# Performance work log

Hardware: AMD Instinct MI355X
Metric: run time of the kernel (lower is better)

The kernel has to match this reference:

```python
import jax, jax.numpy as jnp
import numpy as np

B = 32; N = 512; SEQ_LEN = 8
L = 0.05; T_REF = 5.0; V_TH = 20.0; V_RES = 0.0
SQL = float(np.sqrt(L))
BN_EPS = 1e-5

# ---- Dawson-style lookup tables for the LIF moment activation (built once, float64) ----
_XG = np.linspace(-10.0, 4.0, 7001)
_DX = _XG[1] - _XG[0]

def _cumtrapz(y):
    return np.concatenate([[0.0], np.cumsum(0.5 * (y[1:] + y[:-1]) * _DX)])

_phi = np.exp(-_XG ** 2)
_I = np.exp(-100.0) / 20.0 + _cumtrapz(_phi)          # int_{-inf}^x e^{-t^2} dt (asymptotic tail at -10)
_g = np.exp(_XG ** 2) * _I                             # 1st Dawson-like function g(x)
_G = _cumtrapz(_g)                                     # int g dx (rel. to -10)
_h = np.exp(_XG ** 2) * _cumtrapz(_phi * _g ** 2)      # 2nd Dawson-like function h(x)
_H = _cumtrapz(_h)                                     # int h dx

XG = jnp.asarray(_XG, jnp.float32)
GT = jnp.asarray(_g, jnp.float32)
GI = jnp.asarray(_G, jnp.float32)
HI = jnp.asarray(_H, jnp.float32)

def _interp(x, tab):
    return jnp.interp(x, XG, tab)

def moment_activate(u, s, rho):
    # Mnn_Activate_Mean / Std / Corr: LIF moment activation
    s = jnp.maximum(s, 1e-6)
    ub = jnp.clip((V_TH * L - u) / (s * SQL), -10.0, 4.0)
    lb = jnp.clip((V_RES * L - u) / (s * SQL), -10.0, 4.0)
    dG = _interp(ub, GI) - _interp(lb, GI)
    ua = 1.0 / (T_REF + (2.0 / L) * dG)                               # mean firing rate
    dH = jnp.maximum(_interp(ub, HI) - _interp(lb, HI), 0.0)
    sa = jnp.sqrt((8.0 / L ** 2) * dH * ua ** 3)                      # firing std
    dg = _interp(ub, GT) - _interp(lb, GT)
    chi = ua ** 2 * (2.0 / L) * dg / (SQL * jnp.maximum(sa, 1e-9))    # linear response coeff
    eye = jnp.eye(rho.shape[-1], dtype=rho.dtype)
    rho_out = chi[:, :, None] * chi[:, None, :] * rho                 # [B,N,N]
    rho_out = rho_out * (1.0 - eye) + eye                             # unit diagonal
    return ua, sa, rho_out

def linear_corr(W, b, u, s, rho):
    # Mnn_Linear_Corr: mean via affine map, covariance via W C W^T
    u_out = u @ W.T + b
    Cin = rho * s[:, :, None] * s[:, None, :]                         # [B,N,N] covariance
    C = jnp.einsum('bik,lk->bil', jnp.einsum('ij,bjk->bik', W, Cin), W)
    var = jnp.clip(jnp.diagonal(C, axis1=1, axis2=2), 0.0, None)
    s_out = jnp.sqrt(var)
    denom = s_out[:, :, None] * s_out[:, None, :]
    rho_out = jnp.where(denom > 1e-12, C / jnp.maximum(denom, 1e-12), 0.0)
    return u_out, s_out, rho_out

def mexi_hat(n, k=0.3):
    dx = 2.0 * np.pi / n
    x = np.arange(0.0, 2.0 * np.pi, dx)[:n]
    y = np.exp(2.0 * (np.cos(x) - 1.0)) * np.cos(2.0 * x)
    j = np.arange(n)
    idx = (j[None, :] - j[:, None]) % n                               # w[i,:] = y.roll(i)
    return y[idx].astype(np.float32)

def setup_inputs() -> dict:
    ks = jax.random.split(jax.random.key(0), 10)
    u = jax.random.normal(ks[0], (B, N), jnp.float32)
    s = jax.random.uniform(ks[1], (B, N), jnp.float32, 0.1, 1.0)
    A = jax.random.normal(ks[2], (B, N, N), jnp.float32) / np.sqrt(N)
    sym = 0.5 * (A + jnp.swapaxes(A, 1, 2))
    eye = jnp.eye(N, dtype=jnp.float32)
    rho = jnp.clip(sym, -0.5, 0.5) * (1.0 - eye) + eye                # valid-ish corr matrix
    u_ext = jax.random.normal(ks[3], (B, N), jnp.float32)
    s_ext = jax.random.uniform(ks[4], (B, N), jnp.float32, 0.1, 1.0)
    W = 0.02 * jax.random.normal(ks[5], (N, N), jnp.float32) + 0.1 * jnp.asarray(mexi_hat(N))
    b = 0.02 * jax.random.normal(ks[6], (N,), jnp.float32)
    W_ext = 0.02 * jax.random.normal(ks[7], (N, N), jnp.float32)
    b_ext = 0.02 * jax.random.normal(ks[8], (N,), jnp.float32)
    w_mean = 2.5 * jnp.ones((N,), jnp.float32)
    b_mean = 2.5 * jnp.ones((N,), jnp.float32)
    w_mean_ext = 2.5 * jnp.ones((N,), jnp.float32)
    b_mean_ext = 2.5 * jnp.ones((N,), jnp.float32)
    return {'u': u, 's': s, 'rho': rho, 'u_ext': u_ext, 's_ext': s_ext,
            'W': W, 'b': b, 'W_ext': W_ext, 'b_ext': b_ext,
            'w_mean': w_mean, 'b_mean': b_mean,
            'w_mean_ext': w_mean_ext, 'b_mean_ext': b_mean_ext,
            'seq_len': SEQ_LEN}

def reference(u, s, rho, u_ext, s_ext, W, b, W_ext, b_ext,
              w_mean, b_mean, w_mean_ext, b_mean_ext, seq_len):
    # external pathway (Mnn_Linear_without_Corr + BN), computed once
    u_e = u_ext @ W_ext.T + b_ext
    s_e = jnp.sqrt((s_ext ** 2) @ (W_ext ** 2).T)
    mean_e = jnp.mean(u_e, axis=0); var_e = jnp.var(u_e, axis=0)
    f_e = w_mean_ext / jnp.sqrt(var_e + BN_EPS)
    s_e = s_e * jnp.abs(f_e)                                          # Mnn_Std_Bn1d (uses pre-BN stats)
    u_e = (u_e - mean_e) * f_e + b_mean_ext

    def step(carry, _):
        u, s, rho = carry
        u, s, rho = linear_corr(W, b, u, s, rho)
        mean = jnp.mean(u, axis=0); var = jnp.var(u, axis=0)
        f = w_mean / jnp.sqrt(var + BN_EPS)
        s = s * jnp.abs(f)
        u = (u - mean) * f + b_mean
        u = u + u_e
        s = jnp.sqrt(s * s + s_e * s_e)
        return moment_activate(u, s, rho), None

    (u, s, rho), _ = jax.lax.scan(step, (u, s, rho), None, length=seq_len)
    return u, s, rho
```

## Files before the change

kernel.cpp:

```cpp
#include <hip/hip_runtime.h>
#include <math.h>


#define BB 32
#define NN 512
#define SEQ 8
#define TG 7001

typedef float f32x4 __attribute__((ext_vector_type(4)));
typedef short s16x8 __attribute__((ext_vector_type(8)));

#define GL16(g, l) __builtin_amdgcn_global_load_lds( \
    (const __attribute__((address_space(1))) void*)(g), \
    (__attribute__((address_space(3))) void*)(l), 16, 0, 0)

__device__ __forceinline__ unsigned short bf16_rne(float v) {
    unsigned u = __float_as_uint(v);
    u += 0x7FFFu + ((u >> 16) & 1u);
    return (unsigned short)(u >> 16);
}
__device__ __forceinline__ float bf16_f(unsigned short h) {
    return __uint_as_float(((unsigned)h) << 16);
}
__device__ __forceinline__ void split2(float v, unsigned short& h, unsigned short& l) {
    unsigned short hh = bf16_rne(v);
    h = hh;
    l = bf16_rne(v - bf16_f(hh));
}

__device__ __forceinline__ float interp_tab(const float* __restrict__ tab, float x) {
    float t = (x + 10.0f) * 500.0f;
    t = fminf(fmaxf(t, 0.0f), 7000.0f);
    int i0 = (int)t;
    if (i0 > 6999) i0 = 6999;
    float fr = t - (float)i0;
    float a = tab[i0];
    float b = tab[i0 + 1];
    return a + fr * (b - a);
}

__global__ void k_exp(double* __restrict__ expP, double* __restrict__ expM) {
    int k = blockIdx.x * 256 + threadIdx.x;
    if (k >= TG) return;
    double x = -10.0 + (14.0 / 7000.0) * k;
    expP[k] = exp(x * x);
    expM[k] = exp(-x * x);
}

__device__ double blk_exscan(double part, double* wsum) {
    int t = threadIdx.x, lane = t & 63, wid = t >> 6;
    double run = part;
    #pragma unroll
    for (int off = 1; off < 64; off <<= 1) {
        double nv = __shfl_up(run, off);
        if (lane >= off) run += nv;
    }
    if (lane == 63) wsum[wid] = run;
    __syncthreads();
    if (t < 16) {
        double v = wsum[t];
        #pragma unroll
        for (int off = 1; off < 16; off <<= 1) {
            double nv = __shfl_up(v, off);
            if (lane >= off) v += nv;
        }
        wsum[t] = v;
    }
    __syncthreads();
    double base = (wid > 0) ? wsum[wid - 1] : 0.0;
    double ex = base + run - part;
    __syncthreads();
    return ex;
}

__global__ __launch_bounds__(1024)
void k_scan(const double* __restrict__ expP, const double* __restrict__ expM,
            float* __restrict__ GT, float* __restrict__ GI, float* __restrict__ HI) {
    __shared__ double ys[7008];
    __shared__ double wsum[16];
    const int t = threadIdx.x;
    const double dx = 14.0 / 7000.0;
    int k0 = t * 7, k1 = k0 + 7;
    if (k1 > TG) k1 = TG;
    if (k0 > TG) k0 = TG;
    int kls = (k0 < 1) ? 1 : k0;

    for (int k = k0; k < k1; ++k) ys[k] = expM[k];
    __syncthreads();

    double tmp[7];
    {
        double part = 0.0;
        for (int k = kls; k < k1; ++k) part += 0.5 * (ys[k - 1] + ys[k]) * dx;
        double run = blk_exscan(part, wsum) + exp(-100.0) / 20.0;
        int c = 0;
        for (int k = k0; k < k1; ++k) {
            if (k >= 1) run += 0.5 * (ys[k - 1] + ys[k]) * dx;
            tmp[c] = expP[k] * run;
            GT[k] = (float)tmp[c];
            ++c;
        }
        __syncthreads();
        c = 0;
        for (int k = k0; k < k1; ++k) ys[k] = tmp[c++];
        __syncthreads();
    }
    {
        double part = 0.0;
        for (int k = kls; k < k1; ++k) part += 0.5 * (ys[k - 1] + ys[k]) * dx;
        double run = blk_exscan(part, wsum);
        for (int k = k0; k < k1; ++k) {
            if (k >= 1) run += 0.5 * (ys[k - 1] + ys[k]) * dx;
            GI[k] = (float)run;
        }
        __syncthreads();
    }
    {
        double part = 0.0;
        for (int k = kls; k < k1; ++k) {
            double ya = expM[k - 1] * ys[k - 1] * ys[k - 1];
            double yb = expM[k] * ys[k] * ys[k];
            part += 0.5 * (ya + yb) * dx;
        }
        double run = blk_exscan(part, wsum);
        int c = 0;
        for (int k = k0; k < k1; ++k) {
            if (k >= 1) {
                double ya = expM[k - 1] * ys[k - 1] * ys[k - 1];
                double yb = expM[k] * ys[k] * ys[k];
                run += 0.5 * (ya + yb) * dx;
            }
            tmp[c++] = run;
        }
        __syncthreads();
        c = 0;
        for (int k = k0; k < k1; ++k) ys[k] = tmp[c++];
        __syncthreads();
    }
    {
        double part = 0.0;
        for (int k = kls; k < k1; ++k)
            part += 0.5 * (expP[k - 1] * ys[k - 1] + expP[k] * ys[k]) * dx;
        double run = blk_exscan(part, wsum);
        for (int k = k0; k < k1; ++k) {
            if (k >= 1) run += 0.5 * (expP[k - 1] * ys[k - 1] + expP[k] * ys[k]) * dx;
            HI[k] = (float)run;
        }
    }
}

__global__ void k_splitW(const float* __restrict__ W,
                         unsigned short* __restrict__ Wh, unsigned short* __restrict__ Wl) {
    int idx = blockIdx.x * 256 + threadIdx.x;
    unsigned short h, l;
    split2(W[idx], h, l);
    Wh[idx] = h; Wl[idx] = l;
}

__global__ void k_splitQ(const float* __restrict__ rho, const float* __restrict__ s,
                         unsigned short* __restrict__ Qh, unsigned short* __restrict__ Ql) {
    size_t idx = (size_t)blockIdx.x * 256 + threadIdx.x;
    int b = (int)(idx >> 18);
    int i = (int)((idx >> 9) & 511);
    int j = (int)(idx & 511);
    float v = rho[idx] * s[b * NN + i] * s[b * NN + j];
    unsigned short h, l;
    split2(v, h, l);
    Qh[idx] = h; Ql[idx] = l;
}

template <int PHASE>
__global__ __launch_bounds__(256)
void gemm_step(const unsigned short* __restrict__ Ah, const unsigned short* __restrict__ Al,
               long aStride,
               const unsigned short* __restrict__ Bh, const unsigned short* __restrict__ Bl,
               long bStride,
               unsigned short* __restrict__ Oh, unsigned short* __restrict__ Ol,
               float* __restrict__ Of,
               const float* __restrict__ Wf, float* __restrict__ sv_a, float* __restrict__ sv_b,
               const float* __restrict__ u_prev, const float* __restrict__ bvec,
               float* __restrict__ u_lin,
               const float* __restrict__ bn_w, const float* __restrict__ bmv,
               const float* __restrict__ u_e, const float* __restrict__ s_e2,
               const float* __restrict__ GT, const float* __restrict__ GI,
               const float* __restrict__ HI,
               float* __restrict__ u_next, float* __restrict__ s_next) {
    __shared__ __align__(16) unsigned short As0[8192], As1[8192], Bs0[8192], Bs1[8192];
    __shared__ float slS[256], chS[256], snS[256];

    const int id = blockIdx.x;
    const int member = (id >> 3) & 3;
    const int g = (id & 7) | ((id >> 5) << 3);
    const int p = g & 3;
    const int b = g >> 2;
    const int xt = (PHASE == 0) ? p : member;
    const int yt = (PHASE == 0) ? member : p;
    const int i0 = yt * 128, j0 = xt * 128;
    const int tid = threadIdx.x;
    const int w = tid >> 6, lane = tid & 63;
    const int wqm = w >> 1, wqn = w & 1;

    const unsigned short* Abh = Ah + (size_t)b * aStride;
    const unsigned short* Abl = Al + (size_t)b * aStride;
    const unsigned short* Bbh = Bh + (size_t)b * bStride;
    const unsigned short* Bbl = Bl + (size_t)b * bStride;

    const size_t lgoff = ((size_t)(lane >> 3) * NN) + (size_t)(((lane & 7) ^ (lane >> 3)) << 3);

    auto stage = [&](int k0) {
        #pragma unroll
        for (int inst = 0; inst < 4; ++inst) {
            const int br = w * 32 + inst * 8;
            GL16(Abh + (size_t)(i0 + br) * NN + k0 + lgoff, As0 + br * 64);
            GL16(Abl + (size_t)(i0 + br) * NN + k0 + lgoff, As1 + br * 64);
            GL16(Bbh + (size_t)(j0 + br) * NN + k0 + lgoff, Bs0 + br * 64);
            GL16(Bbl + (size_t)(j0 + br) * NN + k0 + lgoff, Bs1 + br * 64);
        }
    };
    stage(0);

    if (PHASE == 0) {
        if (xt == 0) {
            const int row = i0 + (tid >> 1);
            const int half = tid & 1;
            const float4* wr = (const float4*)(Wf + (size_t)row * NN + half * 256);
            const float4* ur = (const float4*)(u_prev + b * NN + half * 256);
            float a0 = 0.f, a1 = 0.f, a2 = 0.f, a3 = 0.f;
            #pragma unroll 8
            for (int kk = 0; kk < 64; ++kk) {
                float4 wv = wr[kk], uv = ur[kk];
                a0 = fmaf(wv.x, uv.x, a0);
                a1 = fmaf(wv.y, uv.y, a1);
                a2 = fmaf(wv.z, uv.z, a2);
                a3 = fmaf(wv.w, uv.w, a3);
            }
            float au = (a0 + a1) + (a2 + a3);
            au += __shfl_xor(au, 1);
            if (half == 0) u_lin[b * NN + row] = au + bvec[row];
        }
    } else {
        const int ii = (tid < 128) ? (i0 + tid) : (j0 + tid - 128);
        float m = 0.0f;
        for (int bb = 0; bb < BB; ++bb) m += u_lin[bb * NN + ii];
        m *= (1.0f / BB);
        float v = 0.0f;
        for (int bb = 0; bb < BB; ++bb) {
            float d = u_lin[bb * NN + ii] - m;
            v = fmaf(d, d, v);
        }
        v *= (1.0f / BB);
        float f = bn_w[ii] / sqrtf(v + 1e-5f);
        const int idx = b * NN + ii;
        float s_l = sqrtf(fmaxf(sv_a[idx], 0.0f));
        float un = (u_lin[idx] - m) * f + bmv[ii] + u_e[idx];
        float sn = sqrtf(s_l * s_l * f * f + s_e2[idx]);
        const float SQL = 0.22360679774997896f;
        float ss = fmaxf(sn, 1e-6f);
        float inv = 1.0f / (ss * SQL);
        float ubx = fminf(fmaxf((1.0f - un) * inv, -10.0f), 4.0f);
        float lbx = fminf(fmaxf((0.0f - un) * inv, -10.0f), 4.0f);
        float dG = interp_tab(GI, ubx) - interp_tab(GI, lbx);
        float ua = 1.0f / (5.0f + 40.0f * dG);
        float dH = fmaxf(interp_tab(HI, ubx) - interp_tab(HI, lbx), 0.0f);
        float sa = sqrtf(3200.0f * dH * ua * ua * ua);
        float dg2 = interp_tab(GT, ubx) - interp_tab(GT, lbx);
        float ch = ua * ua * 40.0f * dg2 / (SQL * fmaxf(sa, 1e-9f));
        slS[tid] = s_l;
        chS[tid] = ch;
        snS[tid] = sa;
        if (i0 == j0 && tid < 128) {
            u_next[idx] = ua;
            s_next[idx] = sa;
            sv_b[idx] = 0.0f;
        }
    }
    __syncthreads();

    f32x4 acc[4][4];
    #pragma unroll
    for (int m2 = 0; m2 < 4; ++m2)
        #pragma unroll
        for (int n2 = 0; n2 < 4; ++n2) acc[m2][n2] = (f32x4){0.f, 0.f, 0.f, 0.f};

    for (int k0 = 0;;) {
        #pragma unroll
        for (int s = 0; s < 2; ++s) {
            s16x8 ahf[4], alf[4], bhf[4], blf[4];
            #pragma unroll
            for (int t = 0; t < 4; ++t) {
                const int ra = wqm * 64 + t * 16 + (lane & 15);
                const int ao = ra * 64 + ((((lane >> 4) + s * 4) ^ (ra & 7)) << 3);
                ahf[t] = *reinterpret_cast<const s16x8*>(&As0[ao]);
                alf[t] = *reinterpret_cast<const s16x8*>(&As1[ao]);
                const int rb = wqn * 64 + t * 16 + (lane & 15);
                const int bo = rb * 64 + ((((lane >> 4) + s * 4) ^ (rb & 7)) << 3);
                bhf[t] = *reinterpret_cast<const s16x8*>(&Bs0[bo]);
                blf[t] = *reinterpret_cast<const s16x8*>(&Bs1[bo]);
            }
            #pragma unroll
            for (int m2 = 0; m2 < 4; ++m2)
                #pragma unroll
                for (int n2 = 0; n2 < 4; ++n2) {
                    acc[m2][n2] = __builtin_amdgcn_mfma_f32_16x16x32_bf16(ahf[m2], bhf[n2], acc[m2][n2], 0, 0, 0);
                    acc[m2][n2] = __builtin_amdgcn_mfma_f32_16x16x32_bf16(ahf[m2], blf[n2], acc[m2][n2], 0, 0, 0);
                    acc[m2][n2] = __builtin_amdgcn_mfma_f32_16x16x32_bf16(alf[m2], bhf[n2], acc[m2][n2], 0, 0, 0);
                }
        }
        k0 += 64;
        if (k0 >= NN) break;
        __syncthreads();
        stage(k0);
        __syncthreads();
    }

    const size_t bofs = (size_t)b * NN * NN;

    if (PHASE == 0) {
        const int rb0 = i0 + wqm * 64 + (lane >> 4) * 4;
        const int cb0 = j0 + wqn * 64 + (lane & 15);
        float dp[16];
        #pragma unroll
        for (int m2 = 0; m2 < 4; ++m2)
            #pragma unroll
            for (int r = 0; r < 4; ++r) {
                int row = rb0 + m2 * 16 + r;
                const float* wrow = Wf + ((size_t)row << 9) + cb0;
                float s = 0.0f;
                #pragma unroll
                for (int n2 = 0; n2 < 4; ++n2) s = fmaf(acc[m2][n2][r], wrow[n2 * 16], s);
                dp[m2 * 4 + r] = s;
            }
        #pragma unroll
        for (int k = 0; k < 16; ++k) {
            #pragma unroll
            for (int off = 1; off < 16; off <<= 1) dp[k] += __shfl_xor(dp[k], off);
        }
        if ((lane & 15) == 0) {
            #pragma unroll
            for (int k = 0; k < 16; ++k) {
                int row = rb0 + (k >> 2) * 16 + (k & 3);
                atomicAdd(&sv_a[b * NN + row], dp[k]);
            }
        }
        #pragma unroll
        for (int m2 = 0; m2 < 4; ++m2)
            #pragma unroll
            for (int n2 = 0; n2 < 4; ++n2) {
                int col = cb0 + n2 * 16;
                #pragma unroll
                for (int r = 0; r < 4; ++r) {
                    int row = rb0 + m2 * 16 + r;
                    size_t idx = bofs + ((size_t)row << 9) + col;
                    unsigned short h, l;
                    split2(acc[m2][n2][r], h, l);
                    Oh[idx] = h; Ol[idx] = l;
                }
            }
    } else {
        const int lrb = wqm * 64 + (lane >> 4) * 4;
        const int lcb = wqn * 64 + (lane & 15);
        #pragma unroll
        for (int m2 = 0; m2 < 4; ++m2)
            #pragma unroll
            for (int r = 0; r < 4; ++r) {
                const int lr = lrb + m2 * 16 + r;
                const float si = slS[lr], ci = chS[lr], qi = snS[lr];
                const int row = i0 + lr;
                #pragma unroll
                for (int n2 = 0; n2 < 4; ++n2) {
                    const int lc = lcb + n2 * 16;
                    const float sj = slS[128 + lc], cj = chS[128 + lc], qj = snS[128 + lc];
                    const int col = j0 + lc;
                    float denom = si * sj;
                    float rv = (denom > 1e-12f) ? (acc[m2][n2][r] / fmaxf(denom, 1e-12f)) : 0.0f;
                    rv *= ci * cj;
                    if (row == col) rv = 1.0f;
                    size_t idx = bofs + ((size_t)row << 9) + col;
                    if (PHASE == 1) {
                        unsigned short h, l;
                        split2(rv * qi * qj, h, l);
                        Oh[idx] = h; Ol[idx] = l;
                    } else {
                        Of[idx] = rv;
                    }
                }
            }
    }
}

__global__ void k_ext_dots(const float* __restrict__ Wx, const float* __restrict__ bx,
                           const float* __restrict__ ux, const float* __restrict__ sx,
                           float* __restrict__ u_e, float* __restrict__ s_e2) {
    int gw = (blockIdx.x << 2) + (threadIdx.x >> 6);
    int lane = threadIdx.x & 63;
    int b = gw >> 9, i = gw & 511;
    const float* wr = Wx + (size_t)i * NN;
    const float* ub = ux + b * NN;
    const float* sb = sx + b * NN;
    float au = 0.0f, as2 = 0.0f;
    for (int j = lane; j < NN; j += 64) {
        float w = wr[j];
        float s = sb[j];
        au = fmaf(w, ub[j], au);
        as2 = fmaf(w * w, s * s, as2);
    }
    #pragma unroll
    for (int off = 32; off; off >>= 1) {
        au += __shfl_down(au, off);
        as2 += __shfl_down(as2, off);
    }
    if (lane == 0) {
        u_e[b * NN + i] = au + bx[i];
        s_e2[b * NN + i] = as2;
    }
}

__global__ void k_ext_stats(float* __restrict__ u_e, float* __restrict__ s_e2,
                            const float* __restrict__ wmx, const float* __restrict__ bmx) {
    int i = blockIdx.x * blockDim.x + threadIdx.x;
    if (i >= NN) return;
    float m = 0.0f;
    for (int b = 0; b < BB; ++b) m += u_e[b * NN + i];
    m *= (1.0f / BB);
    float v = 0.0f;
    for (int b = 0; b < BB; ++b) {
        float d = u_e[b * NN + i] - m;
        v = fmaf(d, d, v);
    }
    v *= (1.0f / BB);
    float f = wmx[i] / sqrtf(v + 1e-5f);
    float bm = bmx[i];
    for (int b = 0; b < BB; ++b) {
        u_e[b * NN + i] = (u_e[b * NN + i] - m) * f + bm;
        s_e2[b * NN + i] *= f * f;
    }
}

extern "C" void kernel_launch(void* const* d_in, const int* in_sizes, int n_in,
                              void* d_out, int out_size, void* d_ws, size_t ws_size,
                              hipStream_t stream) {
    (void)in_sizes; (void)n_in; (void)out_size; (void)ws_size;
    const float* u_in       = (const float*)d_in[0];
    const float* s_in       = (const float*)d_in[1];
    const float* rho_in     = (const float*)d_in[2];
    const float* u_ext      = (const float*)d_in[3];
    const float* s_ext      = (const float*)d_in[4];
    const float* W          = (const float*)d_in[5];
    const float* bvec       = (const float*)d_in[6];
    const float* W_ext      = (const float*)d_in[7];
    const float* b_ext      = (const float*)d_in[8];
    const float* w_mean     = (const float*)d_in[9];
    const float* b_mean     = (const float*)d_in[10];
    const float* w_mean_ext = (const float*)d_in[11];
    const float* b_mean_ext = (const float*)d_in[12];

    float* out_u   = (float*)d_out;
    float* out_s   = out_u + BB * NN;
    float* out_rho = out_s + BB * NN;
    unsigned short* Qh = (unsigned short*)out_rho;
    unsigned short* Ql = Qh + (size_t)BB * NN * NN;

    char* base = (char*)d_ws;
    size_t off = 0;
    auto alloc = [&](size_t bytes) -> char* {
        char* ptr = base + off;
        off += (bytes + 255) & ~(size_t)255;
        return ptr;
    };
    unsigned short* T1h = (unsigned short*)alloc((size_t)BB * NN * NN * 2);
    unsigned short* T1l = (unsigned short*)alloc((size_t)BB * NN * NN * 2);
    unsigned short* Wh  = (unsigned short*)alloc((size_t)NN * NN * 2);
    unsigned short* Wl  = (unsigned short*)alloc((size_t)NN * NN * 2);
    double* expP = (double*)alloc(TG * 8);
    double* expM = (double*)alloc(TG * 8);
    float* GTt   = (float*)alloc(TG * 4);
    float* GIt   = (float*)alloc(TG * 4);
    float* HIt   = (float*)alloc(TG * 4);
    float* u_e   = (float*)alloc(BB * NN * 4);
    float* s_e2  = (float*)alloc(BB * NN * 4);
    float* uA    = (float*)alloc(BB * NN * 4);
    float* uB2   = (float*)alloc(BB * NN * 4);
    float* sA    = (float*)alloc(BB * NN * 4);
    float* sB2   = (float*)alloc(BB * NN * 4);
    float* u_lin = (float*)alloc(BB * NN * 4);
    float* sv0   = (float*)alloc(BB * NN * 4);
    float* sv1   = (float*)alloc(BB * NN * 4);

    k_exp<<<28, 256, 0, stream>>>(expP, expM);
    k_scan<<<1, 1024, 0, stream>>>(expP, expM, GTt, GIt, HIt);
    k_splitW<<<NN * NN / 256, 256, 0, stream>>>(W, Wh, Wl);
    k_splitQ<<<BB * NN * NN / 256, 256, 0, stream>>>(rho_in, s_in, Qh, Ql);
    k_ext_dots<<<BB * NN / 4, 256, 0, stream>>>(W_ext, b_ext, u_ext, s_ext, u_e, s_e2);
    k_ext_stats<<<2, 256, 0, stream>>>(u_e, s_e2, w_mean_ext, b_mean_ext);
    (void)hipMemsetAsync(sv0, 0, BB * NN * 4, stream);

    const float* cu = u_in;

    for (int t = 0; t < SEQ; ++t) {
        float* sva = (t & 1) ? sv1 : sv0;
        float* svb = (t & 1) ? sv0 : sv1;
        gemm_step<0><<<512, 256, 0, stream>>>(
            Wh, Wl, 0L, Qh, Ql, (long)NN * NN, T1h, T1l, nullptr,
            W, sva, nullptr, cu, bvec, u_lin,
            nullptr, nullptr, nullptr, nullptr, nullptr, nullptr, nullptr,
            nullptr, nullptr);
        float* nu = (t == SEQ - 1) ? out_u : ((t & 1) ? uA : uB2);
        float* ns = (t == SEQ - 1) ? out_s : ((t & 1) ? sA : sB2);
        if (t < SEQ - 1) {
            gemm_step<1><<<512, 256, 0, stream>>>(
                T1h, T1l, (long)NN * NN, Wh, Wl, 0L, Qh, Ql, nullptr,
                nullptr, sva, svb, nullptr, nullptr, u_lin,
                w_mean, b_mean, u_e, s_e2, GTt, GIt, HIt, nu, ns);
        } else {
            gemm_step<2><<<512, 256, 0, stream>>>(
                T1h, T1l, (long)NN * NN, Wh, Wl, 0L, nullptr, nullptr, out_rho,
                nullptr, sva, svb, nullptr, nullptr, u_lin,
                w_mean, b_mean, u_e, s_e2, GTt, GIt, HIt, nu, ns);
        }
        cu = nu;
    }
}
```

Measured before the change: 799.3 us.

## Double-buffer LDS K-tiles with prefetch and spread u-matvec across all blocks

The GEMM main loop now splits LDS into two 32-wide K buffers and issues the global-to-LDS load for the next K slice before computing on the current one, so memory latency overlaps MFMA work and one barrier per iteration is removed. The LDS swizzle and stage addressing are rewritten for the 32-element row width. The mean matvec in phase 0, previously done only by xt==0 blocks, is now spread across all 16 tiles with 8 lanes per row and a shuffle reduction, which removes the load imbalance between blocks. The risk is that halving the K step doubles the iteration count, and a single barrier per iteration may not be enough to keep buffer reuse correct.

```diff
diff --git a/kernel.cpp b/kernel.cpp
--- a/kernel.cpp
+++ b/kernel.cpp
@@ -199,45 +199,49 @@
     const int tid = threadIdx.x;
     const int w = tid >> 6, lane = tid & 63;
     const int wqm = w >> 1, wqn = w & 1;
+    const int kg = lane >> 4;
 
     const unsigned short* Abh = Ah + (size_t)b * aStride;
     const unsigned short* Abl = Al + (size_t)b * aStride;
     const unsigned short* Bbh = Bh + (size_t)b * bStride;
     const unsigned short* Bbl = Bl + (size_t)b * bStride;
 
-    const size_t lgoff = ((size_t)(lane >> 3) * NN) + (size_t)(((lane & 7) ^ (lane >> 3)) << 3);
-
-    auto stage = [&](int k0) {
-        #pragma unroll
-        for (int inst = 0; inst < 4; ++inst) {
-            const int br = w * 32 + inst * 8;
-            GL16(Abh + (size_t)(i0 + br) * NN + k0 + lgoff, As0 + br * 64);
-            GL16(Abl + (size_t)(i0 + br) * NN + k0 + lgoff, As1 + br * 64);
-            GL16(Bbh + (size_t)(j0 + br) * NN + k0 + lgoff, Bs0 + br * 64);
-            GL16(Bbl + (size_t)(j0 + br) * NN + k0 + lgoff, Bs1 + br * 64);
+    const size_t lgoff = ((size_t)(lane >> 2) * NN) + (size_t)((((lane & 3) ^ ((lane >> 3) & 3)) << 3));
+    const int cxor = ((kg ^ (((lane & 15) >> 1) & 3)) << 3);
+
+    auto stage = [&](int pp, int k0) {
+        const int bufo = pp * 4096;
+        #pragma unroll
+        for (int inst = 0; inst < 2; ++inst) {
+            const int br = w * 32 + inst * 16;
+            GL16(Abh + (size_t)(i0 + br) * NN + k0 + lgoff, As0 + bufo + br * 32);
+            GL16(Abl + (size_t)(i0 + br) * NN + k0 + lgoff, As1 + bufo + br * 32);
+            GL16(Bbh + (size_t)(j0 + br) * NN + k0 + lgoff, Bs0 + bufo + br * 32);
+            GL16(Bbl + (size_t)(j0 + br) * NN + k0 + lgoff, Bs1 + bufo + br * 32);
         }
     };
-    stage(0);
+    stage(0, 0);
 
     if (PHASE == 0) {
-        if (xt == 0) {
-            const int row = i0 + (tid >> 1);
-            const int half = tid & 1;
-            const float4* wr = (const float4*)(Wf + (size_t)row * NN + half * 256);
-            const float4* ur = (const float4*)(u_prev + b * NN + half * 256);
-            float a0 = 0.f, a1 = 0.f, a2 = 0.f, a3 = 0.f;
-            #pragma unroll 8
-            for (int kk = 0; kk < 64; ++kk) {
-                float4 wv = wr[kk], uv = ur[kk];
-                a0 = fmaf(wv.x, uv.x, a0);
-                a1 = fmaf(wv.y, uv.y, a1);
-                a2 = fmaf(wv.z, uv.z, a2);
-                a3 = fmaf(wv.w, uv.w, a3);
-            }
-            float au = (a0 + a1) + (a2 + a3);
-            au += __shfl_xor(au, 1);
-            if (half == 0) u_lin[b * NN + row] = au + bvec[row];
-        }
+        const int tile16 = yt * 4 + xt;
+        const int row = tile16 * 32 + (tid >> 3);
+        const int seg = tid & 7;
+        const float4* wr = (const float4*)(Wf + (size_t)row * NN + seg * 64);
+        const float4* ur = (const float4*)(u_prev + b * NN + seg * 64);
+        float a0 = 0.f, a1 = 0.f, a2 = 0.f, a3 = 0.f;
+        #pragma unroll
+        for (int kk = 0; kk < 16; ++kk) {
+            float4 wv = wr[kk], uv = ur[kk];
+            a0 = fmaf(wv.x, uv.x, a0);
+            a1 = fmaf(wv.y, uv.y, a1);
+            a2 = fmaf(wv.z, uv.z, a2);
+            a3 = fmaf(wv.w, uv.w, a3);
+        }
+        float au = (a0 + a1) + (a2 + a3);
+        au += __shfl_xor(au, 1);
+        au += __shfl_xor(au, 2);
+        au += __shfl_xor(au, 4);
+        if (seg == 0) u_lin[b * NN + row] = au + bvec[row];
     } else {
         const int ii = (tid < 128) ? (i0 + tid) : (j0 + tid - 128);
         float m = 0.0f;
@@ -282,34 +286,27 @@
         #pragma unroll
         for (int n2 = 0; n2 < 4; ++n2) acc[m2][n2] = (f32x4){0.f, 0.f, 0.f, 0.f};
 
-    for (int k0 = 0;;) {
-        #pragma unroll
-        for (int s = 0; s < 2; ++s) {
-            s16x8 ahf[4], alf[4], bhf[4], blf[4];
+    for (int it = 0; it < 16; ++it) {
+        if (it < 15) stage((it + 1) & 1, (it + 1) * 32);
+        const int bufo = (it & 1) * 4096;
+        s16x8 ahf[4], alf[4], bhf[4], blf[4];
+        #pragma unroll
+        for (int t = 0; t < 4; ++t) {
+            const int ao = bufo + (wqm * 64 + t * 16 + (lane & 15)) * 32 + cxor;
+            ahf[t] = *reinterpret_cast<const s16x8*>(&As0[ao]);
+            alf[t] = *reinterpret_cast<const s16x8*>(&As1[ao]);
+            const int bo = bufo + (wqn * 64 + t * 16 + (lane & 15)) * 32 + cxor;
+            bhf[t] = *reinterpret_cast<const s16x8*>(&Bs0[bo]);
+            blf[t] = *reinterpret_cast<const s16x8*>(&Bs1[bo]);
+        }
+        #pragma unroll
+        for (int m2 = 0; m2 < 4; ++m2)
             #pragma unroll
-            for (int t = 0; t < 4; ++t) {
-                const int ra = wqm * 64 + t * 16 + (lane & 15);
-                const int ao = ra * 64 + ((((lane >> 4) + s * 4) ^ (ra & 7)) << 3);
-                ahf[t] = *reinterpret_cast<const s16x8*>(&As0[ao]);
-                alf[t] = *reinterpret_cast<const s16x8*>(&As1[ao]);
-                const int rb = wqn * 64 + t * 16 + (lane & 15);
-                const int bo = rb * 64 + ((((lane >> 4) + s * 4) ^ (rb & 7)) << 3);
-                bhf[t] = *reinterpret_cast<const s16x8*>(&Bs0[bo]);
-                blf[t] = *reinterpret_cast<const s16x8*>(&Bs1[bo]);
+            for (int n2 = 0; n2 < 4; ++n2) {
+                acc[m2][n2] = __builtin_amdgcn_mfma_f32_16x16x32_bf16(ahf[m2], bhf[n2], acc[m2][n2], 0, 0, 0);
+                acc[m2][n2] = __builtin_amdgcn_mfma_f32_16x16x32_bf16(ahf[m2], blf[n2], acc[m2][n2], 0, 0, 0);
+                acc[m2][n2] = __builtin_amdgcn_mfma_f32_16x16x32_bf16(alf[m2], bhf[n2], acc[m2][n2], 0, 0, 0);
             }
-            #pragma unroll
-            for (int m2 = 0; m2 < 4; ++m2)
-                #pragma unroll
-                for (int n2 = 0; n2 < 4; ++n2) {
-                    acc[m2][n2] = __builtin_amdgcn_mfma_f32_16x16x32_bf16(ahf[m2], bhf[n2], acc[m2][n2], 0, 0, 0);
-                    acc[m2][n2] = __builtin_amdgcn_mfma_f32_16x16x32_bf16(ahf[m2], blf[n2], acc[m2][n2], 0, 0, 0);
-                    acc[m2][n2] = __builtin_amdgcn_mfma_f32_16x16x32_bf16(alf[m2], bhf[n2], acc[m2][n2], 0, 0, 0);
-                }
-        }
-        k0 += 64;
-        if (k0 >= NN) break;
-        __syncthreads();
-        stage(k0);
         __syncthreads();
     }
 
```

Result: no change. 788.1 us (-1.4%).
